# Kernel optimization log

Measured on AMD Instinct MI355X. Metric: run time of the kernel, lower is better.

## Reference

```python
import jax, jax.numpy as jnp
import numpy as np

E = 8            # n_expert
K = 2            # n_expert_per_token
C = 2048         # n_embd
I = 1408         # moe_intermediate_size
IS = I * 2       # shared expert intermediate (n_shared_expert=2)
B, T = 2, 2048


def setup_inputs() -> dict:
    key = jax.random.key(0)
    ks = jax.random.split(key, 9)
    s = 0.02
    return {
        "x": jax.random.normal(ks[0], (B, T, C), dtype=jnp.float32),
        "gate_w": jax.random.normal(ks[1], (E, C), dtype=jnp.float32) * s,
        # expert MLP weights, torch Linear convention (out_features, in_features)
        "w1": jax.random.normal(ks[2], (E, I, C), dtype=jnp.float32) * s,  # fc_1
        "w2": jax.random.normal(ks[3], (E, I, C), dtype=jnp.float32) * s,  # fc_2
        "w3": jax.random.normal(ks[4], (E, C, I), dtype=jnp.float32) * s,  # proj
        # shared expert
        "sw1": jax.random.normal(ks[5], (IS, C), dtype=jnp.float32) * s,
        "sw2": jax.random.normal(ks[6], (IS, C), dtype=jnp.float32) * s,
        "sw3": jax.random.normal(ks[7], (C, IS), dtype=jnp.float32) * s,
    }


def reference(x, gate_w, w1, w2, w3, sw1, sw2, sw3):
    Bq, Tq, Cq = x.shape
    xf = x.reshape(-1, Cq)  # [N, C], N = B*T

    # top-k routing: softmax in fp32, then top-k probs per token
    logits = xf @ gate_w.T                                   # [N, E]
    probs = jax.nn.softmax(logits.astype(jnp.float32), axis=-1)
    topk_p, topk_i = jax.lax.top_k(probs, K)                 # [N, K]
    # combine weights: comb[n, e] = sum_k topk_p[n,k] * (topk_i[n,k] == e)
    comb = (jax.nn.one_hot(topk_i, E, dtype=jnp.float32)
            * topk_p[..., None]).sum(axis=1).astype(x.dtype)  # [N, E]

    # per-expert gated-SiLU MLP (batched over experts via einsum)
    h1 = jnp.einsum('nc,eic->eni', xf, w1)                   # [E, N, I]
    h2 = jnp.einsum('nc,eic->eni', xf, w2)                   # [E, N, I]
    h = jax.nn.silu(h1) * h2
    eo = jnp.einsum('eni,eci->enc', h, w3)                   # [E, N, C]

    # weighted scatter-combine
    y = jnp.einsum('enc,ne->nc', eo, comb).reshape(Bq, Tq, Cq)

    # shared expert on the residual input
    sh = (jax.nn.silu(xf @ sw1.T) * (xf @ sw2.T)) @ sw3.T    # [N, C]
    return y + sh.reshape(Bq, Tq, Cq)
```

## Files before the change

### kernel.cpp

```cpp
#include <hip/hip_runtime.h>
#include <stdint.h>

#define N_TOK 4096
#define CDIM  2048
#define NEXP  8
#define IDIM  1408
#define ISDIM 2816
#define CAP   2048
#define ICAT  2816
#define SCAT  5632

typedef __attribute__((ext_vector_type(8))) short bf16x8;
typedef __attribute__((ext_vector_type(4))) float f32x4;

#define GLOAD16(gp, lp) __builtin_amdgcn_global_load_lds( \
    (const __attribute__((address_space(1))) void*)(gp),  \
    (__attribute__((address_space(3))) void*)(lp), 16, 0, 0)

__device__ __forceinline__ unsigned short f2bf(float f) {
  union { float f; unsigned u; } c; c.f = f;
  return (unsigned short)((c.u + 0x7FFFu + ((c.u >> 16) & 1u)) >> 16);
}
__device__ __forceinline__ float bf2f(unsigned short h) {
  union { unsigned u; float f; } c; c.u = (unsigned)h << 16;
  return c.f;
}

__device__ __forceinline__ int xcd_swizzle(int orig, int nwg) {
  int q = nwg >> 3, r = nwg & 7;
  int xcd = orig & 7, idx = orig >> 3;
  return (xcd < r ? xcd * (q + 1) : r * (q + 1) + (xcd - r) * q) + idx;
}

__global__ __launch_bounds__(256) void cvt_kernel(
    const float* __restrict__ s, unsigned short* __restrict__ d,
    int chunkElems, size_t dstOff, size_t dstStride) {
  size_t z = blockIdx.z;
  size_t i = (size_t)blockIdx.x * 1024 + (size_t)threadIdx.x * 4;
  if (i >= (size_t)chunkElems) return;
  float4 v = *(const float4*)(s + z * chunkElems + i);
  ushort4 o;
  o.x = f2bf(v.x); o.y = f2bf(v.y); o.z = f2bf(v.z); o.w = f2bf(v.w);
  *(ushort4*)(d + z * dstStride + dstOff + i) = o;
}

__global__ __launch_bounds__(64) void routing_kernel(
    const float* __restrict__ x, const float* __restrict__ gw,
    int* __restrict__ counts, int* __restrict__ list,
    int* __restrict__ slot_of, float* __restrict__ wts) {
  const int n = blockIdx.x;
  const int lane = threadIdx.x;
  const float* xr = x + (size_t)n * CDIM;
  float s[NEXP];
#pragma unroll
  for (int e = 0; e < NEXP; e++) s[e] = 0.f;
  for (int c = lane; c < CDIM; c += 64) {
    float xv = xr[c];
#pragma unroll
    for (int e = 0; e < NEXP; e++) s[e] += xv * gw[e * CDIM + c];
  }
#pragma unroll
  for (int e = 0; e < NEXP; e++) {
    float v = s[e];
    for (int o = 32; o > 0; o >>= 1) v += __shfl_down(v, o);
    s[e] = v;
  }
  if (lane == 0) {
    float mx = s[0];
#pragma unroll
    for (int e = 1; e < NEXP; e++) mx = fmaxf(mx, s[e]);
    float p[NEXP], sum = 0.f;
#pragma unroll
    for (int e = 0; e < NEXP; e++) { p[e] = __expf(s[e] - mx); sum += p[e]; }
    int i0 = 0;
#pragma unroll
    for (int e = 1; e < NEXP; e++) if (p[e] > p[i0]) i0 = e;
    int i1 = (i0 == 0) ? 1 : 0;
#pragma unroll
    for (int e = 0; e < NEXP; e++) if (e != i0 && p[e] > p[i1]) i1 = e;
    float inv = 1.f / sum;
    int s0 = atomicAdd(&counts[i0], 1);
    int s1 = atomicAdd(&counts[i1], 1);
    if (s0 < CAP) list[i0 * CAP + s0] = n; else s0 = 0;
    if (s1 < CAP) list[i1 * CAP + s1] = n; else s1 = 0;
    slot_of[n * 2]     = i0 * CAP + s0;
    slot_of[n * 2 + 1] = i1 * CAP + s1;
    wts[n * 2]     = p[i0] * inv;
    wts[n * 2 + 1] = p[i1] * inv;
  }
}

template <int PHASE>
__global__ __launch_bounds__(512) void moe_gemm(
    const unsigned short* __restrict__ xb,
    const unsigned short* __restrict__ swcat,
    const unsigned short* __restrict__ wcat,
    unsigned short* __restrict__ hsp,
    unsigned short* __restrict__ hep,
    const unsigned short* __restrict__ hs,
    const unsigned short* __restrict__ sw3b,
    const unsigned short* __restrict__ he,
    const unsigned short* __restrict__ w3b,
    float* __restrict__ ysf,
    unsigned short* __restrict__ eo,
    const int* __restrict__ list,
    const int* __restrict__ counts) {
  const int z = blockIdx.z;
  const unsigned short *A, *B;
  unsigned short* O = nullptr;
  float* Of = nullptr;
  int Ka, ldo;
  int cnt = 1 << 30;
  const int* lst = nullptr;
  int Mt, Nt;
  if (PHASE == 1) {
    Mt = 8; Nt = 11; Ka = CDIM;
    if (z < 4) {
      int zm = z >> 1, zn = z & 1;
      A = xb + (size_t)zm * 2048 * CDIM;
      B = swcat + (size_t)zn * ISDIM * CDIM;
      O = hsp + (size_t)zm * 2048 * SCAT + (size_t)zn * ISDIM;
      ldo = SCAT;
    } else {
      int e = z - 4;
      cnt = counts[e]; if (cnt > CAP) cnt = CAP;
      lst = list + e * CAP;
      A = xb;
      B = wcat + (size_t)e * ICAT * CDIM;
      O = hep + (size_t)e * CAP * ICAT;
      ldo = ICAT;
    }
  } else {
    Mt = 8; Nt = 8;
    if (z < 2) {
      Ka = ISDIM;
      A = hs + (size_t)z * 2048 * ISDIM;
      B = sw3b;
      Of = ysf + (size_t)z * 2048 * CDIM;
      ldo = CDIM;
    } else {
      int e = z - 2;
      cnt = counts[e]; if (cnt > CAP) cnt = CAP;
      Ka = IDIM;
      A = he + (size_t)e * CAP * IDIM;
      B = w3b + (size_t)e * CDIM * IDIM;
      O = eo + (size_t)e * CAP * CDIM;
      ldo = CDIM;
    }
  }
  const int wg = xcd_swizzle(blockIdx.x, Mt * Nt);
  const int mt = wg % Mt, nt = wg / Mt;
  if (mt * 256 >= cnt) return;

  __shared__ __align__(16) char aLds[2 * 32768];
  __shared__ __align__(16) char bLds[2 * 32768];

  const int tid = threadIdx.x;
  const int srow = tid >> 3;
  const int scol = ((tid & 7) << 4) ^ ((srow & 7) << 4);
  const char* aSrc[4];
  const char* bSrc[4];
#pragma unroll
  for (int j = 0; j < 4; j++) {
    int ar = mt * 256 + j * 64 + srow;
    if (PHASE == 1 && z >= 4) ar = (ar < cnt) ? lst[ar] : lst[0];
    aSrc[j] = (const char*)A + (size_t)ar * Ka * 2 + scol;
    int br = nt * 256 + j * 64 + srow;
    bSrc[j] = (const char*)B + (size_t)br * Ka * 2 + scol;
  }

  auto stage = [&](int bufsel, int kt) {
    size_t kb = (size_t)kt * 128;
    char* ad = aLds + bufsel * 32768 + tid * 16;
    char* bd = bLds + bufsel * 32768 + tid * 16;
#pragma unroll
    for (int j = 0; j < 4; j++) {
      GLOAD16(aSrc[j] + kb, ad + j * 8192);
      GLOAD16(bSrc[j] + kb, bd + j * 8192);
    }
  };

  const int lane = tid & 63, wid = tid >> 6;
  const int wr = wid >> 2, wc = wid & 3;
  const int lrow = lane & 15;
  const int klane = (lane >> 4) << 4;
  const int ar0 = wr * 128 + lrow;
  const int aOff0 = ar0 * 128 + (klane ^ ((ar0 & 7) << 4));
  const int br0 = wc * 64 + lrow;
  const int bOff0 = br0 * 128 + (klane ^ ((br0 & 7) << 4));

  f32x4 acc[8][4];
#pragma unroll
  for (int mf = 0; mf < 8; mf++)
#pragma unroll
    for (int nf = 0; nf < 4; nf++) acc[mf][nf] = (f32x4){0.f, 0.f, 0.f, 0.f};

  stage(0, 0);
  stage(1, 1);
  const int ntk = Ka >> 6;
  for (int t = 0; t < ntk; t++) {
    const char* ab = aLds + (t & 1) * 32768;
    const char* bb = bLds + (t & 1) * 32768;
    if (t == ntk - 1) asm volatile("s_waitcnt vmcnt(0)" ::: "memory");
    else              asm volatile("s_waitcnt vmcnt(8)" ::: "memory");
    __builtin_amdgcn_s_barrier();
#pragma unroll
    for (int kk = 0; kk < 2; kk++) {
      const char* a0 = ab + (aOff0 ^ (kk << 6));
      const char* b0 = bb + (bOff0 ^ (kk << 6));
      bf16x8 af[8], bfr[4];
#pragma unroll
      for (int mf = 0; mf < 8; mf++) af[mf] = *(const bf16x8*)(a0 + mf * 2048);
#pragma unroll
      for (int nf = 0; nf < 4; nf++) bfr[nf] = *(const bf16x8*)(b0 + nf * 2048);
#pragma unroll
      for (int nf = 0; nf < 4; nf++)
#pragma unroll
        for (int mf = 0; mf < 8; mf++)
          acc[mf][nf] = __builtin_amdgcn_mfma_f32_16x16x32_bf16(af[mf], bfr[nf], acc[mf][nf], 0, 0, 0);
    }
    asm volatile("s_waitcnt lgkmcnt(0)" ::: "memory");
    __builtin_amdgcn_s_barrier();
    if (t + 2 < ntk) stage(t & 1, t + 2);
  }

  const int rowb = mt * 256 + wr * 128;
  const int colb = nt * 256 + wc * 64;
  const int r4 = (lane >> 4) * 4;
#pragma unroll
  for (int mf = 0; mf < 8; mf++) {
    int row0 = rowb + mf * 16 + r4;
#pragma unroll
    for (int nf = 0; nf < 4; nf++) {
      int col = colb + nf * 16 + lrow;
#pragma unroll
      for (int r = 0; r < 4; r++) {
        if (PHASE == 2 && z < 2)
          Of[(size_t)(row0 + r) * ldo + col] = acc[mf][nf][r];
        else
          O[(size_t)(row0 + r) * ldo + col] = f2bf(acc[mf][nf][r]);
      }
    }
  }
}

__global__ __launch_bounds__(256) void act_kernel(
    const unsigned short* __restrict__ in, unsigned short* __restrict__ out,
    int I8, int ldi) {
  int c8 = blockIdx.x * 256 + threadIdx.x;
  if (c8 >= I8) return;
  size_t r = blockIdx.y;
  const unsigned short* p = in + r * (size_t)ldi + (size_t)c8 * 8;
  bf16x8 a = *(const bf16x8*)p;
  bf16x8 g = *(const bf16x8*)(p + (size_t)I8 * 8);
  bf16x8 o;
#pragma unroll
  for (int k = 0; k < 8; k++) {
    float zv = bf2f((unsigned short)a[k]);
    float gv = bf2f((unsigned short)g[k]);
    float v = zv / (1.f + __expf(-zv)) * gv;
    o[k] = (short)f2bf(v);
  }
  *(bf16x8*)(out + r * (size_t)(I8 * 8) + (size_t)c8 * 8) = o;
}

__global__ __launch_bounds__(256) void combine_kernel(
    float* __restrict__ y, const float* __restrict__ ysf,
    const unsigned short* __restrict__ eo,
    const int* __restrict__ slot_of, const float* __restrict__ wts) {
  int idx = blockIdx.x * 256 + threadIdx.x;
  int n = idx >> 9;
  int c = (idx & 511) * 4;
  float4 v = *(const float4*)(ysf + (size_t)n * CDIM + c);
#pragma unroll
  for (int k = 0; k < 2; k++) {
    int slot = slot_of[n * 2 + k];
    float w = wts[n * 2 + k];
    ushort4 h = *(const ushort4*)(eo + (size_t)slot * CDIM + c);
    v.x += w * bf2f(h.x);
    v.y += w * bf2f(h.y);
    v.z += w * bf2f(h.z);
    v.w += w * bf2f(h.w);
  }
  *(float4*)(y + (size_t)n * CDIM + c) = v;
}

extern "C" void kernel_launch(void* const* d_in, const int* in_sizes, int n_in,
                              void* d_out, int out_size, void* d_ws, size_t ws_size,
                              hipStream_t stream) {
  const float* x   = (const float*)d_in[0];
  const float* gw  = (const float*)d_in[1];
  const float* w1  = (const float*)d_in[2];
  const float* w2  = (const float*)d_in[3];
  const float* w3  = (const float*)d_in[4];
  const float* sw1 = (const float*)d_in[5];
  const float* sw2 = (const float*)d_in[6];
  const float* sw3 = (const float*)d_in[7];
  float* y = (float*)d_out;

  char* ws = (char*)d_ws;
  size_t off = 0;
  auto alloc = [&](size_t b) -> void* {
    void* p = ws + off;
    off += (b + 255) & ~(size_t)255;
    return p;
  };
  unsigned short* xb    = (unsigned short*)alloc((size_t)N_TOK * CDIM * 2);
  unsigned short* wcat  = (unsigned short*)alloc((size_t)NEXP * ICAT * CDIM * 2);
  unsigned short* w3b   = (unsigned short*)alloc((size_t)NEXP * CDIM * IDIM * 2);
  unsigned short* swcat = (unsigned short*)alloc((size_t)SCAT * CDIM * 2);
  unsigned short* sw3b  = (unsigned short*)alloc((size_t)CDIM * ISDIM * 2);
  unsigned short* hsp   = (unsigned short*)alloc((size_t)N_TOK * SCAT * 2);
  unsigned short* hep   = (unsigned short*)alloc((size_t)NEXP * CAP * ICAT * 2);
  int*   counts  = (int*)alloc(NEXP * 4);
  int*   list    = (int*)alloc((size_t)NEXP * CAP * 4);
  int*   slot_of = (int*)alloc((size_t)N_TOK * 2 * 4);
  float* wtsb    = (float*)alloc((size_t)N_TOK * 2 * 4);
  unsigned short* hs = wcat;
  unsigned short* he = wcat + (size_t)N_TOK * ISDIM;
  float*          ysf = (float*)hsp;
  unsigned short* eoB = hep;

  hipMemsetAsync(counts, 0, NEXP * 4, stream);
  routing_kernel<<<N_TOK, 64, 0, stream>>>(x, gw, counts, list, slot_of, wtsb);

  cvt_kernel<<<dim3(8192, 1, 1), 256, 0, stream>>>(x, xb, N_TOK * CDIM, 0, 0);
  cvt_kernel<<<dim3(2816, 1, NEXP), 256, 0, stream>>>(w1, wcat, IDIM * CDIM, 0, (size_t)ICAT * CDIM);
  cvt_kernel<<<dim3(2816, 1, NEXP), 256, 0, stream>>>(w2, wcat, IDIM * CDIM, (size_t)IDIM * CDIM, (size_t)ICAT * CDIM);
  cvt_kernel<<<dim3(22528, 1, 1), 256, 0, stream>>>(w3, w3b, NEXP * CDIM * IDIM, 0, 0);
  cvt_kernel<<<dim3(5632, 1, 1), 256, 0, stream>>>(sw1, swcat, ISDIM * CDIM, 0, 0);
  cvt_kernel<<<dim3(5632, 1, 1), 256, 0, stream>>>(sw2, swcat, ISDIM * CDIM, (size_t)ISDIM * CDIM, 0);
  cvt_kernel<<<dim3(5632, 1, 1), 256, 0, stream>>>(sw3, sw3b, CDIM * ISDIM, 0, 0);

  moe_gemm<1><<<dim3(88, 1, 12), 512, 0, stream>>>(
      xb, swcat, wcat, hsp, hep, hs, sw3b, he, w3b, ysf, eoB, list, counts);

  act_kernel<<<dim3(2, N_TOK), 256, 0, stream>>>(hsp, hs, ISDIM / 8, SCAT);
  act_kernel<<<dim3(1, NEXP * CAP), 256, 0, stream>>>(hep, he, IDIM / 8, ICAT);

  moe_gemm<2><<<dim3(64, 1, 10), 512, 0, stream>>>(
      xb, swcat, wcat, hsp, hep, hs, sw3b, he, w3b, ysf, eoB, list, counts);

  combine_kernel<<<(N_TOK * (CDIM / 4)) / 256, 256, 0, stream>>>(y, ysf, eoB, slot_of, wtsb);
}
```

Baseline: 686.0 us.

## Split GEMM mainloop into K-half LDS stages with interleaved loads and MFMA quarters

Restructures the GEMM main loop so LDS is split into two K-halves per buffer. Each iteration interleaves LDS fragment reads, staging of the next half-tile, and four MFMA quarter-blocks, with setprio raised around each MFMA burst. The LDS swizzle and stride change to 64-byte rows to match the halves. The aim is to overlap global-to-LDS traffic and LDS reads with matrix math better. In exchange it adds many extra barriers per K-step and makes the vmcnt bookkeeping more delicate.

```diff
diff --git a/kernel.cpp b/kernel.cpp
--- a/kernel.cpp
+++ b/kernel.cpp
@@ -113,6 +113,7 @@
   int cnt = 1 << 30;
   const int* lst = nullptr;
   int Mt, Nt;
+  bool gath = false;
   if (PHASE == 1) {
     Mt = 8; Nt = 11; Ka = CDIM;
     if (z < 4) {
@@ -125,6 +126,7 @@
       int e = z - 4;
       cnt = counts[e]; if (cnt > CAP) cnt = CAP;
       lst = list + e * CAP;
+      gath = true;
       A = xb;
       B = wcat + (size_t)e * ICAT * CDIM;
       O = hep + (size_t)e * CAP * ICAT;
@@ -152,42 +154,39 @@
   const int mt = wg % Mt, nt = wg / Mt;
   if (mt * 256 >= cnt) return;
 
-  __shared__ __align__(16) char aLds[2 * 32768];
-  __shared__ __align__(16) char bLds[2 * 32768];
+  __shared__ __align__(16) char lds[2][2][2][16384];
 
   const int tid = threadIdx.x;
-  const int srow = tid >> 3;
-  const int scol = ((tid & 7) << 4) ^ ((srow & 7) << 4);
-  const char* aSrc[4];
-  const char* bSrc[4];
-#pragma unroll
-  for (int j = 0; j < 4; j++) {
-    int ar = mt * 256 + j * 64 + srow;
-    if (PHASE == 1 && z >= 4) ar = (ar < cnt) ? lst[ar] : lst[0];
-    aSrc[j] = (const char*)A + (size_t)ar * Ka * 2 + scol;
-    int br = nt * 256 + j * 64 + srow;
-    bSrc[j] = (const char*)B + (size_t)br * Ka * 2 + scol;
-  }
-
-  auto stage = [&](int bufsel, int kt) {
-    size_t kb = (size_t)kt * 128;
-    char* ad = aLds + bufsel * 32768 + tid * 16;
-    char* bd = bLds + bufsel * 32768 + tid * 16;
-#pragma unroll
-    for (int j = 0; j < 4; j++) {
-      GLOAD16(aSrc[j] + kb, ad + j * 8192);
-      GLOAD16(bSrc[j] + kb, bd + j * 8192);
-    }
+  const int srow = tid >> 2;
+  const int c16  = (tid & 3) << 4;
+  const int scol = c16 ^ (((srow >> 1) & 3) << 4);
+  const char* aS[2];
+  const char* bS[2];
+#pragma unroll
+  for (int j = 0; j < 2; j++) {
+    int ar = mt * 256 + j * 128 + srow;
+    if (PHASE == 1 && gath) ar = (ar < cnt) ? lst[ar] : lst[0];
+    aS[j] = (const char*)A + (size_t)ar * Ka * 2 + scol;
+    int br = nt * 256 + j * 128 + srow;
+    bS[j] = (const char*)B + (size_t)br * Ka * 2 + scol;
+  }
+  auto stageHalf = [&](int buf, int kt, int h) {
+    size_t kb = (size_t)kt * 128 + (size_t)(h << 6);
+    char* aD = &lds[buf][0][h][0] + tid * 16;
+    char* bD = &lds[buf][1][h][0] + tid * 16;
+    GLOAD16(aS[0] + kb, aD);
+    GLOAD16(aS[1] + kb, aD + 8192);
+    GLOAD16(bS[0] + kb, bD);
+    GLOAD16(bS[1] + kb, bD + 8192);
   };
 
   const int lane = tid & 63, wid = tid >> 6;
   const int wr = wid >> 2, wc = wid & 3;
   const int lrow = lane & 15;
   const int klane = (lane >> 4) << 4;
-  const int ar0 = wr * 128 + lrow;
-  const int aOff0 = ar0 * 128 + (klane ^ ((ar0 & 7) << 4));
-  const int br0 = wc * 64 + lrow;
-  const int bOff0 = br0 * 128 + (klane ^ ((br0 & 7) << 4));
+  const int rsw = ((lrow >> 1) & 3) << 4;
+  const int aOff = (wr * 128 + lrow) * 64 + (klane ^ rsw);
+  const int bOff = (wc * 64 + lrow) * 64 + (klane ^ rsw);
 
   f32x4 acc[8][4];
 #pragma unroll
@@ -195,34 +194,72 @@
 #pragma unroll
     for (int nf = 0; nf < 4; nf++) acc[mf][nf] = (f32x4){0.f, 0.f, 0.f, 0.f};
 
-  stage(0, 0);
-  stage(1, 1);
+  stageHalf(0, 0, 0);
+  stageHalf(0, 0, 1);
+  stageHalf(1, 1, 0);
+  asm volatile("s_waitcnt vmcnt(8)" ::: "memory");
+  __builtin_amdgcn_s_barrier();
+
+#define MFMA_Q(MB)                                                             \
+  _Pragma("unroll")                                                            \
+  for (int nf = 0; nf < 4; nf++)                                               \
+    _Pragma("unroll")                                                          \
+    for (int m = 0; m < 4; m++)                                                \
+      acc[(MB) * 4 + m][nf] = __builtin_amdgcn_mfma_f32_16x16x32_bf16(         \
+          aR[m], bR[nf], acc[(MB) * 4 + m][nf], 0, 0, 0);
+
   const int ntk = Ka >> 6;
   for (int t = 0; t < ntk; t++) {
-    const char* ab = aLds + (t & 1) * 32768;
-    const char* bb = bLds + (t & 1) * 32768;
-    if (t == ntk - 1) asm volatile("s_waitcnt vmcnt(0)" ::: "memory");
-    else              asm volatile("s_waitcnt vmcnt(8)" ::: "memory");
-    __builtin_amdgcn_s_barrier();
-#pragma unroll
-    for (int kk = 0; kk < 2; kk++) {
-      const char* a0 = ab + (aOff0 ^ (kk << 6));
-      const char* b0 = bb + (bOff0 ^ (kk << 6));
-      bf16x8 af[8], bfr[4];
-#pragma unroll
-      for (int mf = 0; mf < 8; mf++) af[mf] = *(const bf16x8*)(a0 + mf * 2048);
-#pragma unroll
-      for (int nf = 0; nf < 4; nf++) bfr[nf] = *(const bf16x8*)(b0 + nf * 2048);
-#pragma unroll
-      for (int nf = 0; nf < 4; nf++)
-#pragma unroll
-        for (int mf = 0; mf < 8; mf++)
-          acc[mf][nf] = __builtin_amdgcn_mfma_f32_16x16x32_bf16(af[mf], bfr[nf], acc[mf][nf], 0, 0, 0);
-    }
+    const int p = t & 1;
+    const char* aK0 = &lds[p][0][0][0];
+    const char* aK1 = &lds[p][0][1][0];
+    const char* bK0 = &lds[p][1][0][0];
+    const char* bK1 = &lds[p][1][1][0];
+    bf16x8 aR[4], bR[4];
+#pragma unroll
+    for (int i = 0; i < 4; i++) aR[i] = *(const bf16x8*)(aK0 + aOff + i * 1024);
+#pragma unroll
+    for (int i = 0; i < 4; i++) bR[i] = *(const bf16x8*)(bK0 + bOff + i * 1024);
+    if (t + 1 < ntk) stageHalf(p ^ 1, t + 1, 1);
+    __builtin_amdgcn_s_barrier();
     asm volatile("s_waitcnt lgkmcnt(0)" ::: "memory");
-    __builtin_amdgcn_s_barrier();
-    if (t + 2 < ntk) stage(t & 1, t + 2);
-  }
+    __builtin_amdgcn_s_setprio(1);
+    MFMA_Q(0)
+    __builtin_amdgcn_s_setprio(0);
+    __builtin_amdgcn_s_barrier();
+#pragma unroll
+    for (int i = 0; i < 4; i++) aR[i] = *(const bf16x8*)(aK0 + aOff + (i + 4) * 1024);
+    if (t + 1 < ntk) asm volatile("s_waitcnt vmcnt(8)" ::: "memory");
+    else             asm volatile("s_waitcnt vmcnt(0)" ::: "memory");
+    __builtin_amdgcn_s_barrier();
+    asm volatile("s_waitcnt lgkmcnt(0)" ::: "memory");
+    __builtin_amdgcn_s_setprio(1);
+    MFMA_Q(1)
+    __builtin_amdgcn_s_setprio(0);
+    __builtin_amdgcn_s_barrier();
+#pragma unroll
+    for (int i = 0; i < 4; i++) aR[i] = *(const bf16x8*)(aK1 + aOff + i * 1024);
+#pragma unroll
+    for (int i = 0; i < 4; i++) bR[i] = *(const bf16x8*)(bK1 + bOff + i * 1024);
+    if (t + 2 < ntk) stageHalf(p, t + 2, 0);
+    __builtin_amdgcn_s_barrier();
+    asm volatile("s_waitcnt lgkmcnt(0)" ::: "memory");
+    __builtin_amdgcn_s_setprio(1);
+    MFMA_Q(0)
+    __builtin_amdgcn_s_setprio(0);
+    __builtin_amdgcn_s_barrier();
+#pragma unroll
+    for (int i = 0; i < 4; i++) aR[i] = *(const bf16x8*)(aK1 + aOff + (i + 4) * 1024);
+    if (t + 2 < ntk)      asm volatile("s_waitcnt vmcnt(8)" ::: "memory");
+    else if (t + 1 < ntk) asm volatile("s_waitcnt vmcnt(4)" ::: "memory");
+    __builtin_amdgcn_s_barrier();
+    asm volatile("s_waitcnt lgkmcnt(0)" ::: "memory");
+    __builtin_amdgcn_s_setprio(1);
+    MFMA_Q(1)
+    __builtin_amdgcn_s_setprio(0);
+    __builtin_amdgcn_s_barrier();
+  }
+#undef MFMA_Q
 
   const int rowb = mt * 256 + wr * 128;
   const int colb = nt * 256 + wc * 64;
```

Result: faster. 669.2 us (-2.5%).
